# Performance work log

Hardware: AMD Instinct MI355X
Metric: run time of the kernel (lower is better)

## Reference

```python
import jax, jax.numpy as jnp
import numpy as np

B, S, HID = 2, 2048, 2048
H, KV, D = 16, 8, 128
EPS = 1e-6
MROPE = [21, 21, 22]  # half_dim=64 -> [64//3, 64//3, 64-2*(64//3)]
SCALE = D ** -0.5


def setup_inputs() -> dict:
    key = jax.random.key(0)
    ks = jax.random.split(key, 8)
    hidden_states = jax.random.normal(ks[0], (B, S, HID), jnp.float32)
    # 3D mrope cos/sin: one position grid per modality axis (use same arange positions)
    inv_freq = 1.0 / (10000.0 ** (jnp.arange(0, D, 2, dtype=jnp.float32) / D))  # [64]
    pos = jnp.arange(S, dtype=jnp.float32)
    freqs = pos[:, None] * inv_freq[None, :]                  # [S, 64]
    emb = jnp.concatenate([freqs, freqs], axis=-1)            # [S, 128]
    cos = jnp.broadcast_to(jnp.cos(emb)[None, None], (3, B, S, D)).astype(jnp.float32)
    sin = jnp.broadcast_to(jnp.sin(emb)[None, None], (3, B, S, D)).astype(jnp.float32)
    q_w = jax.random.normal(ks[1], (H * D, HID), jnp.float32) * 0.02
    k_w = jax.random.normal(ks[2], (KV * D, HID), jnp.float32) * 0.02
    v_w = jax.random.normal(ks[3], (KV * D, HID), jnp.float32) * 0.02
    o_w = jax.random.normal(ks[4], (HID, H * D), jnp.float32) * 0.02
    q_norm_w = jnp.ones((D,), jnp.float32)
    k_norm_w = jnp.ones((D,), jnp.float32)
    return dict(hidden_states=hidden_states, cos=cos, sin=sin, q_w=q_w, k_w=k_w,
                v_w=v_w, o_w=o_w, q_norm_w=q_norm_w, k_norm_w=k_norm_w)


def _rmsnorm(x, w):
    var = jnp.mean(jnp.square(x.astype(jnp.float32)), axis=-1, keepdims=True)
    return (x * jax.lax.rsqrt(var + EPS)).astype(x.dtype) * w


def _rotate_half(x):
    x1, x2 = jnp.split(x, 2, axis=-1)
    return jnp.concatenate([-x2, x1], axis=-1)


def _mrope_mix(t):
    # t: [3, B, S, D]; split last dim into mrope_section*2 chunks, pick chunk i from axis-0 index i%3
    sections = MROPE * 2
    idx = np.cumsum(sections)[:-1]
    chunks = jnp.split(t, idx, axis=-1)
    mixed = jnp.concatenate([c[i % 3] for i, c in enumerate(chunks)], axis=-1)  # [B, S, D]
    return mixed[:, None, :, :]  # unsqueeze head dim -> [B, 1, S, D]


def reference(hidden_states, cos, sin, q_w, k_w, v_w, o_w, q_norm_w, k_norm_w):
    # QKV projections -> [B, n_heads, S, D]
    q = (hidden_states @ q_w.T).reshape(B, S, H, D)
    k = (hidden_states @ k_w.T).reshape(B, S, KV, D)
    v = (hidden_states @ v_w.T).reshape(B, S, KV, D)
    q = _rmsnorm(q, q_norm_w).transpose(0, 2, 1, 3)   # [B, H, S, D]
    k = _rmsnorm(k, k_norm_w).transpose(0, 2, 1, 3)   # [B, KV, S, D]
    v = v.transpose(0, 2, 1, 3)                       # [B, KV, S, D]
    # 3D multimodal RoPE
    c = _mrope_mix(cos)
    s = _mrope_mix(sin)
    q = q * c + _rotate_half(q) * s
    k = k * c + _rotate_half(k) * s
    # GQA: repeat kv heads
    groups = H // KV
    k = jnp.repeat(k, groups, axis=1)  # [B, H, S, D]
    v = jnp.repeat(v, groups, axis=1)
    # causal SDPA (eager)
    scores = jnp.einsum('bhqd,bhkd->bhqk', q, k) * SCALE
    causal = jnp.tril(jnp.ones((S, S), bool))
    scores = jnp.where(causal[None, None], scores, jnp.finfo(scores.dtype).min)
    probs = jax.nn.softmax(scores, axis=-1)
    attn = jnp.einsum('bhqk,bhkd->bhqd', probs, v)     # [B, H, S, D]
    attn = attn.transpose(0, 2, 1, 3).reshape(B, S, H * D)
    return attn @ o_w.T
```

## Files before the change

kernel.cpp:

```cpp
#include <hip/hip_runtime.h>
#include <hip/hip_bf16.h>

typedef __attribute__((ext_vector_type(8))) short short8;
typedef __attribute__((ext_vector_type(4))) short short4v;
typedef __attribute__((ext_vector_type(4))) float f32x4;

#define B_ 2
#define S_ 2048
#define HID_ 2048
#define H_ 16
#define KV_ 8
#define D_ 128
#define SCALE_ 0.08838834764831845f

__device__ inline short f2bf(float f) {
    union { __hip_bfloat16 h; short s; } u;
    u.h = __float2bfloat16(f);
    return u.s;
}
__device__ inline float bf2f(short s) {
    union { short s; __hip_bfloat16 h; } u;
    u.s = s;
    return __bfloat162float(u.h);
}

__device__ inline void gld16(const short* g, short* l) {
    __builtin_amdgcn_global_load_lds(
        (const __attribute__((address_space(1))) unsigned int*)g,
        (__attribute__((address_space(3))) unsigned int*)l, 16, 0, 0);
}

__device__ inline int mrope_axis(int d) {
    int m = d & 63;
    return m < 21 ? 0 : (m < 42 ? 1 : 2);
}
__global__ __launch_bounds__(256) void prep(const float* __restrict__ hid,
                                            const float* __restrict__ qw_,
                                            const float* __restrict__ kw_,
                                            const float* __restrict__ vw_,
                                            const float* __restrict__ ow_,
                                            const float* __restrict__ cosp,
                                            const float* __restrict__ sinp,
                                            short* __restrict__ Hb,
                                            short* __restrict__ Wqkv,
                                            short* __restrict__ Owb,
                                            float* __restrict__ cm,
                                            float* __restrict__ sm) {
    int bid = blockIdx.x;
    if (bid < 20480) {
        const float* src; short* dst; int base;
        if (bid < 8192)       { src = hid; dst = Hb;              base = bid; }
        else if (bid < 12288) { src = qw_; dst = Wqkv;            base = bid - 8192; }
        else if (bid < 14336) { src = kw_; dst = Wqkv + 4194304;  base = bid - 12288; }
        else if (bid < 16384) { src = vw_; dst = Wqkv + 6291456;  base = bid - 14336; }
        else                  { src = ow_; dst = Owb;             base = bid - 16384; }
        int i = base * 1024 + threadIdx.x * 4;
        float4 v = *(const float4*)(&src[i]);
        short4v o;
        o.x = f2bf(v.x); o.y = f2bf(v.y); o.z = f2bf(v.z); o.w = f2bf(v.w);
        *(short4v*)(&dst[i]) = o;
    } else {
        const size_t AX = (size_t)B_ * S_ * D_;
        int i0 = (bid - 20480) * 1024 + threadIdx.x * 4;
#pragma unroll
        for (int k = 0; k < 4; ++k) {
            int idx = i0 + k;
            int d = idx & (D_ - 1);
            size_t src = (size_t)mrope_axis(d) * AX + idx;
            cm[idx] = cosp[src];
            sm[idx] = sinp[src];
        }
    }
}

__global__ __launch_bounds__(256) void gemm_bt(const short* __restrict__ A,
                                               const short* __restrict__ B,
                                               float* __restrict__ C,
                                               int M, int N, int K) {
    __shared__ __align__(16) short As[128 * 64];
    __shared__ __align__(16) short Bs[128 * 64];
    int tid = threadIdx.x;
    int wave = tid >> 6, lane = tid & 63;
    int m16 = lane & 15, quad = lane >> 4;
    int wr = wave >> 1, wc = wave & 1;
    int m0 = blockIdx.y * 128, n0 = blockIdx.x * 128;
    int srow = lane >> 3;
    int scol = ((lane & 7) ^ srow) << 3;
    f32x4 acc[4][4] = {};
    for (int k0 = 0; k0 < K; k0 += 64) {
#pragma unroll
        for (int i = 0; i < 4; ++i) {
            gld16(&A[(size_t)(m0 + wave * 32 + i * 8 + srow) * K + k0 + scol],
                  &As[(wave * 32 + i * 8) * 64]);
            gld16(&B[(size_t)(n0 + wave * 32 + i * 8 + srow) * K + k0 + scol],
                  &Bs[(wave * 32 + i * 8) * 64]);
        }
        __syncthreads();
        short8 a[4][2], b[4][2];
#pragma unroll
        for (int i = 0; i < 4; ++i)
#pragma unroll
            for (int kk = 0; kk < 2; ++kk) {
                int gsw = (((kk << 2) + quad) ^ (m16 & 7)) << 3;
                a[i][kk] = *(const short8*)(&As[(wr * 64 + i * 16 + m16) * 64 + gsw]);
                b[i][kk] = *(const short8*)(&Bs[(wc * 64 + i * 16 + m16) * 64 + gsw]);
            }
#pragma unroll
        for (int kk = 0; kk < 2; ++kk)
#pragma unroll
            for (int i = 0; i < 4; ++i)
#pragma unroll
                for (int j = 0; j < 4; ++j)
                    acc[i][j] = __builtin_amdgcn_mfma_f32_16x16x32_bf16(a[i][kk], b[j][kk],
                                                                        acc[i][j], 0, 0, 0);
        __syncthreads();
    }
#pragma unroll
    for (int i = 0; i < 4; ++i) {
        int row = m0 + wr * 64 + i * 16 + quad * 4;
#pragma unroll
        for (int j = 0; j < 4; ++j) {
            int col = n0 + wc * 64 + j * 16 + m16;
#pragma unroll
            for (int r = 0; r < 4; ++r)
                C[(size_t)(row + r) * N + col] = acc[i][j][r];
        }
    }
}


#define VM2 asm volatile("s_waitcnt vmcnt(2)" ::: "memory")
#define VM0 asm volatile("s_waitcnt vmcnt(0)" ::: "memory")

#define LDA(dst, QI)                                                               \
    _Pragma("unroll") for (int ii = 0; ii < 4; ++ii)                               \
        _Pragma("unroll") for (int kk = 0; kk < 2; ++kk)                           \
            dst[ii][kk] = *(const short8*)&lds[RA +                                \
                (wr * 128 + ((QI) * 4 + ii) * 16 + m16) * 64 +                     \
                ((((kk << 2) + quad) ^ (m16 & 7)) << 3)]

#define LDB(dst, QJ)                                                               \
    _Pragma("unroll") for (int jj = 0; jj < 2; ++jj)                               \
        _Pragma("unroll") for (int kk = 0; kk < 2; ++kk)                           \
            dst[jj][kk] = *(const short8*)&lds[RB +                                \
                ((QJ) * 128 + wc * 32 + jj * 16 + m16) * 64 +                      \
                ((((kk << 2) + quad) ^ (m16 & 7)) << 3)]

#define MM(ua, ub, QI, QJ)                                                         \
    _Pragma("unroll") for (int kk = 0; kk < 2; ++kk)                               \
        _Pragma("unroll") for (int ii = 0; ii < 4; ++ii)                           \
            _Pragma("unroll") for (int jj = 0; jj < 2; ++jj)                       \
                acc[(QI) * 4 + ii][(QJ) * 2 + jj] =                                \
                    __builtin_amdgcn_mfma_f32_16x16x32_bf16(                       \
                        ua[ii][kk], ub[jj][kk],                                    \
                        acc[(QI) * 4 + ii][(QJ) * 2 + jj], 0, 0, 0)

#define STGA(q) do {                                                               \
    int r_ = (wave << 3) + (lane >> 3);                                            \
    int g_ = (lane & 7) ^ (r_ & 7);                                                \
    gld16(&Am[(size_t)(m0 + (q) * 64 + r_) * 2048 + kc + (g_ << 3)],               \
          &lds[PA + (q) * 4096 + (wave << 9)]);                                    \
} while (0)
#define STGB(h, c) do {                                                            \
    int s_ = (wave << 3) + (lane >> 3);                                            \
    int sl_ = (h) * 128 + (c) * 64 + s_;                                           \
    int rr_ = ((sl_ >> 5) & 3) * 64 + (h) * 32 + (sl_ & 31);                       \
    int g_ = (lane & 7) ^ (sl_ & 7);                                               \
    gld16(&Bm[(size_t)(n0 + rr_) * 2048 + kc + (g_ << 3)],                         \
          &lds[PB + ((h) * 128 + (c) * 64) * 64 + (wave << 9)]);                   \
} while (0)

#define PH(LOADS, STG, MFMAS, WAITOP) do {                                         \
    LOADS;                                                                         \
    STG;                                                                           \
    __builtin_amdgcn_sched_barrier(0);                                             \
    __builtin_amdgcn_s_barrier();                                                  \
    asm volatile("s_waitcnt lgkmcnt(0)" ::: "memory");                             \
    __builtin_amdgcn_sched_barrier(0);                                             \
    __builtin_amdgcn_s_setprio(1);                                                 \
    MFMAS;                                                                         \
    __builtin_amdgcn_s_setprio(0);                                                 \
    WAITOP;                                                                        \
    __builtin_amdgcn_sched_barrier(0);                                             \
    __builtin_amdgcn_s_barrier();                                                  \
} while (0)

__global__ __launch_bounds__(512, 2) void qkv_fused(const short* __restrict__ Am,
                                                    const short* __restrict__ Bm,
                                                    const float* __restrict__ qnw,
                                                    const float* __restrict__ knw,
                                                    const float* __restrict__ cm,
                                                    const float* __restrict__ sm,
                                                    short* __restrict__ Qb,
                                                    short* __restrict__ Kb,
                                                    short* __restrict__ Vb) {
    __shared__ __align__(16) char smem[131072];
    short* lds = (short*)smem;
    int tid = threadIdx.x;
    int wave = tid >> 6, lane = tid & 63;
    int m16 = lane & 15, quad = lane >> 4;
    int wr = wave >> 2, wc = wave & 3;
    int m0 = blockIdx.y * 256, n0 = blockIdx.x * 256;
    f32x4 acc[8][4] = {};

    {
        const int kc = 0, PA = 0, PB = 16384;
        STGA(0); STGA(1); STGA(2); STGA(3);
        STGB(0, 0); STGB(0, 1); STGB(1, 0); STGB(1, 1);
        asm volatile("s_waitcnt vmcnt(0)" ::: "memory");
        __builtin_amdgcn_sched_barrier(0);
        __builtin_amdgcn_s_barrier();
    }

    short8 af[4][2], bfX[2][2], bfY[2][2];
    for (int t = 0; t < 31; ++t) {
        const int RA = (t & 1) << 15, RB = RA + 16384;
        const int PA = RA ^ 32768, PB = PA + 16384;
        const int kc = (t + 1) << 6;
        PH({ LDA(af, 0); LDB(bfX, 0); }, { STGA(0); STGA(2); },       MM(af, bfX, 0, 0), VM2);
        PH({ LDB(bfY, 1); },             { STGB(0, 0); STGB(0, 1); }, MM(af, bfY, 0, 1), );
        PH({ LDA(af, 1); },              { STGB(1, 0); STGB(1, 1); }, MM(af, bfY, 1, 1), );
        PH({ ; },                        { STGA(1); STGA(3); },       MM(af, bfX, 1, 0), VM2);
    }
    {
        const int RA = 32768, RB = RA + 16384;
        PH({ LDA(af, 0); LDB(bfX, 0); }, { ; }, MM(af, bfX, 0, 0), VM0);
        PH({ LDB(bfY, 1); },             { ; }, MM(af, bfY, 0, 1), );
        PH({ LDA(af, 1); },              { ; }, MM(af, bfY, 1, 1), );
        PH({ ; },                        { ; }, MM(af, bfX, 1, 0), );
    }

    int bb = m0 >> 11, s0 = m0 & (S_ - 1);
    int x = blockIdx.x;
    if (x >= 12) {
        short* T = (short*)smem;
        int kv0 = (x - 12) << 1;
        for (int hs = 0; hs < 2; ++hs) {
            __syncthreads();
            if (wr == hs) {
#pragma unroll
                for (int i = 0; i < 8; ++i)
#pragma unroll
                    for (int j = 0; j < 4; ++j) {
                        short4v v4;
#pragma unroll
                        for (int r = 0; r < 4; ++r) v4[r] = f2bf(acc[i][j][r]);
                        *(short4v*)&T[(wc * 64 + j * 16 + m16) * 136 + i * 16 + quad * 4] = v4;
                    }
            }
            __syncthreads();
#pragma unroll
            for (int it = 0; it < 8; ++it) {
                int e = (it * 512 + tid) * 8;
                int col = e >> 7, ro = e & 127;
                int kvh = col >> 7, d = col & 127;
                *(short8*)&Vb[(((size_t)(bb * KV_ + kv0 + kvh)) * D_ + d) * S_ +
                              s0 + hs * 128 + ro] =
                    *(const short8*)&T[col * 136 + ro];
            }
        }
    } else {
        short* T = (short*)smem;
        float* part = (float*)(smem + 67584);
        float* rsL  = (float*)(smem + 69632);
        const float* nw = (x < 8) ? qnw : knw;
        int hbase = (x < 8) ? (x << 1) : ((x - 8) << 1);
        short* obase = (x < 8) ? (Qb + ((size_t)bb * H_ + hbase) * S_ * D_)
                               : (Kb + ((size_t)bb * KV_ + hbase) * S_ * D_);
        for (int hs = 0; hs < 2; ++hs) {
            __syncthreads();
            if (wr == hs) {
#pragma unroll
                for (int i = 0; i < 8; ++i)
#pragma unroll
                    for (int r = 0; r < 4; ++r) {
                        float t = acc[i][0][r] * acc[i][0][r] + acc[i][1][r] * acc[i][1][r]
                                + acc[i][2][r] * acc[i][2][r] + acc[i][3][r] * acc[i][3][r];
#pragma unroll
                        for (int msk = 8; msk >= 1; msk >>= 1) t += __shfl_xor(t, msk, 64);
                        if (m16 == 0) part[wc * 128 + i * 16 + quad * 4 + r] = t;
                    }
#pragma unroll
                for (int i = 0; i < 8; ++i)
#pragma unroll
                    for (int j = 0; j < 4; ++j)
#pragma unroll
                        for (int r = 0; r < 4; ++r)
                            T[(i * 16 + quad * 4 + r) * 264 + wc * 64 + j * 16 + m16] =
                                f2bf(acc[i][j][r]);
            }
            __syncthreads();
            if (tid < 256) {
                int row = tid >> 1, hh = tid & 1;
                float tot = part[hh * 256 + row] + part[hh * 256 + 128 + row];
                rsL[tid] = rsqrtf(tot * (1.0f / 128.0f) + 1e-6f);
            }
            __syncthreads();
#pragma unroll
            for (int it = 0; it < 8; ++it) {
                int e = (it * 512 + tid) * 8;
                int row = e >> 8, c = e & 255;
                int hh = c >> 7, colc = c & 127;
                int pcol = colc ^ 64;
                int srow = s0 + hs * 128 + row;
                float rsv = rsL[row * 2 + hh];
                float sg = (colc < 64) ? -1.f : 1.f;
                short8 nv = *(const short8*)&T[row * 264 + c];
                short8 pv = *(const short8*)&T[row * 264 + hh * 128 + pcol];
                size_t cmb = ((size_t)(bb * S_ + srow)) * D_ + colc;
                float4 cA = *(const float4*)&cm[cmb];
                float4 cB = *(const float4*)&cm[cmb + 4];
                float4 sA = *(const float4*)&sm[cmb];
                float4 sB = *(const float4*)&sm[cmb + 4];
                float4 wA = *(const float4*)&nw[colc];
                float4 wB = *(const float4*)&nw[colc + 4];
                float4 wpA = *(const float4*)&nw[pcol];
                float4 wpB = *(const float4*)&nw[pcol + 4];
                float cs[8] = {cA.x, cA.y, cA.z, cA.w, cB.x, cB.y, cB.z, cB.w};
                float sn[8] = {sA.x, sA.y, sA.z, sA.w, sB.x, sB.y, sB.z, sB.w};
                float wv[8] = {wA.x, wA.y, wA.z, wA.w, wB.x, wB.y, wB.z, wB.w};
                float wp[8] = {wpA.x, wpA.y, wpA.z, wpA.w, wpB.x, wpB.y, wpB.z, wpB.w};
                short8 o;
#pragma unroll
                for (int k = 0; k < 8; ++k) {
                    float xv = bf2f(nv[k]) * rsv * wv[k];
                    float pvv = bf2f(pv[k]) * rsv * wp[k];
                    o[k] = f2bf(xv * cs[k] + sg * pvv * sn[k]);
                }
                *(short8*)&(obase + (size_t)hh * S_ * D_)[(size_t)srow * D_ + colc] = o;
            }
        }
    }
}

#undef PH
#undef LDA
#undef LDB
#undef MM
#undef STGA
#undef STGB
#undef VM2
#undef VM0

#define KPAD 136
#define VPAD 72
__global__ __launch_bounds__(256) void attn_fa(const short* __restrict__ Qb,
                                               const short* __restrict__ Kb,
                                               const short* __restrict__ Vb,
                                               short* __restrict__ Ab) {
    __shared__ __align__(16) short Ks[64 * KPAD];
    __shared__ __align__(16) short Vs[128 * VPAD];
    __shared__ __align__(16) short Ps[4][16 * VPAD];
    int tid = threadIdx.x;
    int wave = tid >> 6, lane = tid & 63;
    int m16 = lane & 15, quad = lane >> 4;
    int bh = blockIdx.x;
    int h = bh & 15, b = bh >> 4;
    int qt = 31 - blockIdx.y;
    int kv = h >> 1;
    const short* Qp = Qb + (size_t)(b * H_ + h) * S_ * D_;
    const short* Kp = Kb + (size_t)(b * KV_ + kv) * S_ * D_;
    const short* Vp = Vb + (size_t)(b * KV_ + kv) * D_ * S_;
    int q_base = qt * 64 + wave * 16;
    int qrow = q_base + m16;
    short8 qf[4];
#pragma unroll
    for (int c = 0; c < 4; ++c)
        qf[c] = *(const short8*)(&Qp[(size_t)(q_base + m16) * D_ + c * 32 + quad * 8]);
    f32x4 o_acc[8] = {};
    float m_r = -1e30f, l_r = 0.f;
    int nchunks = qt + 1;
    for (int kc = 0; kc < nchunks; ++kc) {
        int k0 = kc * 64;
#pragma unroll
        for (int it = 0; it < 4; ++it) {
            int cc = tid + it * 256;
            int row = cc >> 4, col = (cc & 15) * 8;
            *(uint4*)(&Ks[row * KPAD + col]) = *(const uint4*)(&Kp[(size_t)(k0 + row) * D_ + col]);
        }
#pragma unroll
        for (int it = 0; it < 4; ++it) {
            int cc = tid + it * 256;
            int row = cc >> 3, col = (cc & 7) * 8;
            *(uint4*)(&Vs[row * VPAD + col]) = *(const uint4*)(&Vp[(size_t)row * S_ + k0 + col]);
        }
        __syncthreads();
        float sv[4][4];
#pragma unroll
        for (int nt = 0; nt < 4; ++nt) {
            f32x4 facc = {};
#pragma unroll
            for (int c = 0; c < 4; ++c) {
                short8 kfr = *(const short8*)(&Ks[(nt * 16 + m16) * KPAD + c * 32 + quad * 8]);
                facc = __builtin_amdgcn_mfma_f32_16x16x32_bf16(kfr, qf[c], facc, 0, 0, 0);
            }
            if (kc == qt) {
#pragma unroll
                for (int r = 0; r < 4; ++r) {
                    int key = k0 + nt * 16 + quad * 4 + r;
                    sv[nt][r] = (key <= qrow) ? facc[r] * SCALE_ : -1e30f;
                }
            } else {
#pragma unroll
                for (int r = 0; r < 4; ++r) sv[nt][r] = facc[r] * SCALE_;
            }
        }
        float mx = -1e30f;
#pragma unroll
        for (int nt = 0; nt < 4; ++nt)
#pragma unroll
            for (int r = 0; r < 4; ++r) mx = fmaxf(mx, sv[nt][r]);
        mx = fmaxf(mx, __shfl_xor(mx, 16, 64));
        mx = fmaxf(mx, __shfl_xor(mx, 32, 64));
        float m_new = fmaxf(m_r, mx);
        float alpha = __expf(m_r - m_new);
        float p[4][4], sum = 0.f;
#pragma unroll
        for (int nt = 0; nt < 4; ++nt)
#pragma unroll
            for (int r = 0; r < 4; ++r) { p[nt][r] = __expf(sv[nt][r] - m_new); sum += p[nt][r]; }
        sum += __shfl_xor(sum, 16, 64);
        sum += __shfl_xor(sum, 32, 64);
        l_r = l_r * alpha + sum;
        m_r = m_new;
#pragma unroll
        for (int j = 0; j < 8; ++j) {
            f32x4 t = o_acc[j];
#pragma unroll
            for (int r = 0; r < 4; ++r) t[r] *= alpha;
            o_acc[j] = t;
        }
#pragma unroll
        for (int nt = 0; nt < 4; ++nt) {
            short4v pk;
#pragma unroll
            for (int r = 0; r < 4; ++r) pk[r] = f2bf(p[nt][r]);
            *(short4v*)&Ps[wave][m16 * VPAD + nt * 16 + quad * 4] = pk;
        }
#pragma unroll
        for (int kk = 0; kk < 2; ++kk) {
            short8 pf = *(const short8*)(&Ps[wave][m16 * VPAD + kk * 32 + quad * 8]);
#pragma unroll
            for (int j = 0; j < 8; ++j) {
                short8 vfr = *(const short8*)(&Vs[(j * 16 + m16) * VPAD + kk * 32 + quad * 8]);
                o_acc[j] = __builtin_amdgcn_mfma_f32_16x16x32_bf16(vfr, pf, o_acc[j], 0, 0, 0);
            }
        }
        __syncthreads();
    }
    float inv_l = 1.0f / l_r;
    size_t base = ((size_t)(b * S_ + qrow)) * (H_ * D_) + h * D_;
#pragma unroll
    for (int j = 0; j < 8; ++j) {
        short4v ov;
#pragma unroll
        for (int r = 0; r < 4; ++r) ov[r] = f2bf(o_acc[j][r] * inv_l);
        *(short4v*)&Ab[base + j * 16 + quad * 4] = ov;
    }
}

extern "C" void kernel_launch(void* const* d_in, const int* in_sizes, int n_in,
                              void* d_out, int out_size, void* d_ws, size_t ws_size,
                              hipStream_t stream) {
    const float* hid  = (const float*)d_in[0];
    const float* cosp = (const float*)d_in[1];
    const float* sinp = (const float*)d_in[2];
    const float* q_w  = (const float*)d_in[3];
    const float* k_w  = (const float*)d_in[4];
    const float* v_w  = (const float*)d_in[5];
    const float* o_w  = (const float*)d_in[6];
    const float* qnw  = (const float*)d_in[7];
    const float* knw  = (const float*)d_in[8];

    char* w = (char*)d_ws;
    short* Hb    = (short*)w;  w += (size_t)4096 * 2048 * 2;
    short* Wqkv  = (short*)w;  w += (size_t)4096 * 2048 * 2;
    short* Owb   = (short*)w;  w += (size_t)2048 * 2048 * 2;
    short* Qb    = (short*)w;  w += (size_t)B_ * H_ * S_ * D_ * 2;
    short* Kb    = (short*)w;  w += (size_t)B_ * KV_ * S_ * D_ * 2;
    short* Vb    = (short*)w;  w += (size_t)B_ * KV_ * D_ * S_ * 2;
    short* Ab    = (short*)w;  w += (size_t)4096 * 2048 * 2;
    float* cos_m = (float*)w;  w += (size_t)B_ * S_ * D_ * 4;
    float* sin_m = (float*)w;  w += (size_t)B_ * S_ * D_ * 4;

    prep<<<20992, 256, 0, stream>>>(hid, q_w, k_w, v_w, o_w, cosp, sinp,
                                    Hb, Wqkv, Owb, cos_m, sin_m);

    qkv_fused<<<dim3(16, 16), 512, 0, stream>>>(Hb, Wqkv, qnw, knw, cos_m, sin_m,
                                                Qb, Kb, Vb);

    attn_fa<<<dim3(32, 32), 256, 0, stream>>>(Qb, Kb, Vb, Ab);

    gemm_bt<<<dim3(16, 32), 256, 0, stream>>>(Ab, Owb, (float*)d_out, 4096, 2048, 2048);
}
```

Before: 353.1 us.

## Split QKV epilogue into separate kernel, swizzle blocks, double-buffer attention K/V

The QKV GEMM no longer does RMSNorm and RoPE in its epilogue. It writes bf16 Q/K columns to a scratch buffer, and a new qkv_post kernel applies norm and rotary. The GEMM also gets a block-index swizzle for L2 locality, relaxed vmcnt waits, and drops the occupancy-2 launch bound. Attention now double-buffers K/V tiles with async global-to-LDS loads into XOR-swizzled LDS and raises priority around the MFMA sections. The tradeoff is an extra kernel launch and an extra write and read of a 4096x3072 intermediate.

After: 329.6 us. 6.7% less time.

```diff
diff --git a/kernel.cpp b/kernel.cpp
--- a/kernel.cpp
+++ b/kernel.cpp
@@ -129,6 +129,7 @@
 }
 
 
+#define VM4 asm volatile("s_waitcnt vmcnt(4)" ::: "memory")
 #define VM2 asm volatile("s_waitcnt vmcnt(2)" ::: "memory")
 #define VM0 asm volatile("s_waitcnt vmcnt(0)" ::: "memory")
 
@@ -185,29 +186,28 @@
     __builtin_amdgcn_s_barrier();                                                  \
 } while (0)
 
-__global__ __launch_bounds__(512, 2) void qkv_fused(const short* __restrict__ Am,
-                                                    const short* __restrict__ Bm,
-                                                    const float* __restrict__ qnw,
-                                                    const float* __restrict__ knw,
-                                                    const float* __restrict__ cm,
-                                                    const float* __restrict__ sm,
-                                                    short* __restrict__ Qb,
-                                                    short* __restrict__ Kb,
-                                                    short* __restrict__ Vb) {
+__global__ __launch_bounds__(512) void gemm_qkv(const short* __restrict__ Am,
+                                                const short* __restrict__ Bm,
+                                                short* __restrict__ Cq,
+                                                short* __restrict__ Vb) {
     __shared__ __align__(16) char smem[131072];
     short* lds = (short*)smem;
     int tid = threadIdx.x;
     int wave = tid >> 6, lane = tid & 63;
     int m16 = lane & 15, quad = lane >> 4;
     int wr = wave >> 2, wc = wave & 3;
-    int m0 = blockIdx.y * 256, n0 = blockIdx.x * 256;
+    int orig = blockIdx.y * 16 + blockIdx.x;
+    int swz = (orig & 7) * 32 + (orig >> 3);
+    int bx = swz & 15, by = swz >> 4;
+    int m0 = by * 256, n0 = bx * 256;
+    int x = bx;
     f32x4 acc[8][4] = {};
 
     {
         const int kc = 0, PA = 0, PB = 16384;
         STGA(0); STGA(1); STGA(2); STGA(3);
         STGB(0, 0); STGB(0, 1); STGB(1, 0); STGB(1, 1);
-        asm volatile("s_waitcnt vmcnt(0)" ::: "memory");
+        VM0;
         __builtin_amdgcn_sched_barrier(0);
         __builtin_amdgcn_s_barrier();
     }
@@ -217,21 +217,20 @@
         const int RA = (t & 1) << 15, RB = RA + 16384;
         const int PA = RA ^ 32768, PB = PA + 16384;
         const int kc = (t + 1) << 6;
-        PH({ LDA(af, 0); LDB(bfX, 0); }, { STGA(0); STGA(2); },       MM(af, bfX, 0, 0), VM2);
-        PH({ LDB(bfY, 1); },             { STGB(0, 0); STGB(0, 1); }, MM(af, bfY, 0, 1), );
-        PH({ LDA(af, 1); },              { STGB(1, 0); STGB(1, 1); }, MM(af, bfY, 1, 1), );
-        PH({ ; },                        { STGA(1); STGA(3); },       MM(af, bfX, 1, 0), VM2);
+        PH({ LDA(af, 0); LDB(bfX, 0); }, { STGA(0); STGA(2); },       MM(af, bfX, 0, 0), VM4);
+        PH({ LDB(bfY, 1); },             { STGB(0, 0); STGB(0, 1); }, MM(af, bfY, 0, 1), VM4);
+        PH({ LDA(af, 1); },              { STGB(1, 0); STGB(1, 1); }, MM(af, bfY, 1, 1), VM4);
+        PH({ ; },                        { STGA(1); STGA(3); },       MM(af, bfX, 1, 0), VM4);
     }
     {
         const int RA = 32768, RB = RA + 16384;
-        PH({ LDA(af, 0); LDB(bfX, 0); }, { ; }, MM(af, bfX, 0, 0), VM0);
-        PH({ LDB(bfY, 1); },             { ; }, MM(af, bfY, 0, 1), );
+        PH({ LDA(af, 0); LDB(bfX, 0); }, { ; }, MM(af, bfX, 0, 0), VM2);
+        PH({ LDB(bfY, 1); },             { ; }, MM(af, bfY, 0, 1), VM0);
         PH({ LDA(af, 1); },              { ; }, MM(af, bfY, 1, 1), );
         PH({ ; },                        { ; }, MM(af, bfX, 1, 0), );
     }
 
     int bb = m0 >> 11, s0 = m0 & (S_ - 1);
-    int x = blockIdx.x;
     if (x >= 12) {
         short* T = (short*)smem;
         int kv0 = (x - 12) << 1;
@@ -260,74 +259,15 @@
             }
         }
     } else {
-        short* T = (short*)smem;
-        float* part = (float*)(smem + 67584);
-        float* rsL  = (float*)(smem + 69632);
-        const float* nw = (x < 8) ? qnw : knw;
-        int hbase = (x < 8) ? (x << 1) : ((x - 8) << 1);
-        short* obase = (x < 8) ? (Qb + ((size_t)bb * H_ + hbase) * S_ * D_)
-                               : (Kb + ((size_t)bb * KV_ + hbase) * S_ * D_);
-        for (int hs = 0; hs < 2; ++hs) {
-            __syncthreads();
-            if (wr == hs) {
-#pragma unroll
-                for (int i = 0; i < 8; ++i)
-#pragma unroll
-                    for (int r = 0; r < 4; ++r) {
-                        float t = acc[i][0][r] * acc[i][0][r] + acc[i][1][r] * acc[i][1][r]
-                                + acc[i][2][r] * acc[i][2][r] + acc[i][3][r] * acc[i][3][r];
-#pragma unroll
-                        for (int msk = 8; msk >= 1; msk >>= 1) t += __shfl_xor(t, msk, 64);
-                        if (m16 == 0) part[wc * 128 + i * 16 + quad * 4 + r] = t;
-                    }
-#pragma unroll
-                for (int i = 0; i < 8; ++i)
-#pragma unroll
-                    for (int j = 0; j < 4; ++j)
-#pragma unroll
-                        for (int r = 0; r < 4; ++r)
-                            T[(i * 16 + quad * 4 + r) * 264 + wc * 64 + j * 16 + m16] =
-                                f2bf(acc[i][j][r]);
-            }
-            __syncthreads();
-            if (tid < 256) {
-                int row = tid >> 1, hh = tid & 1;
-                float tot = part[hh * 256 + row] + part[hh * 256 + 128 + row];
-                rsL[tid] = rsqrtf(tot * (1.0f / 128.0f) + 1e-6f);
-            }
-            __syncthreads();
-#pragma unroll
-            for (int it = 0; it < 8; ++it) {
-                int e = (it * 512 + tid) * 8;
-                int row = e >> 8, c = e & 255;
-                int hh = c >> 7, colc = c & 127;
-                int pcol = colc ^ 64;
-                int srow = s0 + hs * 128 + row;
-                float rsv = rsL[row * 2 + hh];
-                float sg = (colc < 64) ? -1.f : 1.f;
-                short8 nv = *(const short8*)&T[row * 264 + c];
-                short8 pv = *(const short8*)&T[row * 264 + hh * 128 + pcol];
-                size_t cmb = ((size_t)(bb * S_ + srow)) * D_ + colc;
-                float4 cA = *(const float4*)&cm[cmb];
-                float4 cB = *(const float4*)&cm[cmb + 4];
-                float4 sA = *(const float4*)&sm[cmb];
-                float4 sB = *(const float4*)&sm[cmb + 4];
-                float4 wA = *(const float4*)&nw[colc];
-                float4 wB = *(const float4*)&nw[colc + 4];
-                float4 wpA = *(const float4*)&nw[pcol];
-                float4 wpB = *(const float4*)&nw[pcol + 4];
-                float cs[8] = {cA.x, cA.y, cA.z, cA.w, cB.x, cB.y, cB.z, cB.w};
-                float sn[8] = {sA.x, sA.y, sA.z, sA.w, sB.x, sB.y, sB.z, sB.w};
-                float wv[8] = {wA.x, wA.y, wA.z, wA.w, wB.x, wB.y, wB.z, wB.w};
-                float wp[8] = {wpA.x, wpA.y, wpA.z, wpA.w, wpB.x, wpB.y, wpB.z, wpB.w};
-                short8 o;
-#pragma unroll
-                for (int k = 0; k < 8; ++k) {
-                    float xv = bf2f(nv[k]) * rsv * wv[k];
-                    float pvv = bf2f(pv[k]) * rsv * wp[k];
-                    o[k] = f2bf(xv * cs[k] + sg * pvv * sn[k]);
-                }
-                *(short8*)&(obase + (size_t)hh * S_ * D_)[(size_t)srow * D_ + colc] = o;
+#pragma unroll
+        for (int i = 0; i < 8; ++i) {
+            int row = m0 + wr * 128 + i * 16 + quad * 4;
+#pragma unroll
+            for (int j = 0; j < 4; ++j) {
+                int col = n0 + wc * 64 + j * 16 + m16;
+#pragma unroll
+                for (int r = 0; r < 4; ++r)
+                    Cq[(size_t)(row + r) * 3072 + col] = f2bf(acc[i][j][r]);
             }
         }
     }
@@ -339,17 +279,84 @@
 #undef MM
 #undef STGA
 #undef STGB
+#undef VM4
 #undef VM2
 #undef VM0
 
-#define KPAD 136
+#define TP 136
+__global__ __launch_bounds__(256) void qkv_post(const short* __restrict__ Cq,
+                                                const float* __restrict__ qnw,
+                                                const float* __restrict__ knw,
+                                                const float* __restrict__ cm,
+                                                const float* __restrict__ sm,
+                                                short* __restrict__ Qb,
+                                                short* __restrict__ Kb) {
+    __shared__ __align__(16) short T[128 * TP];
+    __shared__ float sq[128];
+    __shared__ float rsA[128];
+    int tid = threadIdx.x;
+    int hk = blockIdx.x;
+    int m0 = blockIdx.y * 128;
+    int b = m0 >> 11, s0 = m0 & (S_ - 1);
+#pragma unroll
+    for (int it = 0; it < 8; ++it) {
+        int idx = it * 256 + tid;
+        int row = idx >> 4, g = idx & 15;
+        short8 v = *(const short8*)&Cq[(size_t)(m0 + row) * 3072 + hk * 128 + g * 8];
+        *(short8*)&T[row * TP + g * 8] = v;
+        float s = 0.f;
+#pragma unroll
+        for (int k = 0; k < 8; ++k) { float f = bf2f(v[k]); s += f * f; }
+#pragma unroll
+        for (int msk = 8; msk >= 1; msk >>= 1) s += __shfl_xor(s, msk, 64);
+        if ((tid & 15) == 0) sq[row] = s;
+    }
+    __syncthreads();
+    if (tid < 128) rsA[tid] = rsqrtf(sq[tid] * (1.0f / 128.0f) + 1e-6f);
+    __syncthreads();
+    const float* nw = (hk < 16) ? qnw : knw;
+    short* outp = (hk < 16) ? (Qb + ((size_t)(b * H_ + hk)) * S_ * D_)
+                            : (Kb + ((size_t)(b * KV_ + hk - 16)) * S_ * D_);
+    size_t cmb = ((size_t)(b * S_ + s0)) * D_;
+#pragma unroll
+    for (int it = 0; it < 8; ++it) {
+        int e = (it * 256 + tid) * 8;
+        int row = e >> 7, colc = e & 127;
+        int pc = colc ^ 64;
+        float rs = rsA[row];
+        float sg = (colc < 64) ? -1.f : 1.f;
+        short8 nv = *(const short8*)&T[row * TP + colc];
+        short8 pv = *(const short8*)&T[row * TP + pc];
+        float4 cA = *(const float4*)&cm[cmb + (size_t)row * D_ + colc];
+        float4 cB = *(const float4*)&cm[cmb + (size_t)row * D_ + colc + 4];
+        float4 sA = *(const float4*)&sm[cmb + (size_t)row * D_ + colc];
+        float4 sB = *(const float4*)&sm[cmb + (size_t)row * D_ + colc + 4];
+        float4 wA = *(const float4*)&nw[colc];
+        float4 wB = *(const float4*)&nw[colc + 4];
+        float4 wpA = *(const float4*)&nw[pc];
+        float4 wpB = *(const float4*)&nw[pc + 4];
+        float cs[8] = {cA.x, cA.y, cA.z, cA.w, cB.x, cB.y, cB.z, cB.w};
+        float sn[8] = {sA.x, sA.y, sA.z, sA.w, sB.x, sB.y, sB.z, sB.w};
+        float wv[8] = {wA.x, wA.y, wA.z, wA.w, wB.x, wB.y, wB.z, wB.w};
+        float wp[8] = {wpA.x, wpA.y, wpA.z, wpA.w, wpB.x, wpB.y, wpB.z, wpB.w};
+        short8 o;
+#pragma unroll
+        for (int k = 0; k < 8; ++k) {
+            float xv = bf2f(nv[k]) * rs * wv[k];
+            float pvv = bf2f(pv[k]) * rs * wp[k];
+            o[k] = f2bf(xv * cs[k] + sg * pvv * sn[k]);
+        }
+        *(short8*)&outp[(size_t)(s0 + row) * D_ + colc] = o;
+    }
+}
+
 #define VPAD 72
 __global__ __launch_bounds__(256) void attn_fa(const short* __restrict__ Qb,
                                                const short* __restrict__ Kb,
                                                const short* __restrict__ Vb,
                                                short* __restrict__ Ab) {
-    __shared__ __align__(16) short Ks[64 * KPAD];
-    __shared__ __align__(16) short Vs[128 * VPAD];
+    __shared__ __align__(16) short Ks[2][64 * 128];
+    __shared__ __align__(16) short Vs[2][128 * 64];
     __shared__ __align__(16) short Ps[4][16 * VPAD];
     int tid = threadIdx.x;
     int wave = tid >> 6, lane = tid & 63;
@@ -370,28 +377,52 @@
     f32x4 o_acc[8] = {};
     float m_r = -1e30f, l_r = 0.f;
     int nchunks = qt + 1;
+
+#pragma unroll
+    for (int j = 0; j < 4; ++j) {
+        int idx = wave * 4 + j;
+        int r = idx * 4 + (lane >> 4);
+        int g = (lane & 15) ^ (r & 7);
+        gld16(&Kp[(size_t)r * D_ + g * 8], &Ks[0][idx * 512]);
+    }
+#pragma unroll
+    for (int j = 0; j < 4; ++j) {
+        int idx = wave * 4 + j;
+        int r = idx * 8 + (lane >> 3);
+        int g = (lane & 7) ^ (r & 7);
+        gld16(&Vp[(size_t)r * S_ + g * 8], &Vs[0][idx * 512]);
+    }
+    __syncthreads();
+
     for (int kc = 0; kc < nchunks; ++kc) {
         int k0 = kc * 64;
-#pragma unroll
-        for (int it = 0; it < 4; ++it) {
-            int cc = tid + it * 256;
-            int row = cc >> 4, col = (cc & 15) * 8;
-            *(uint4*)(&Ks[row * KPAD + col]) = *(const uint4*)(&Kp[(size_t)(k0 + row) * D_ + col]);
-        }
-#pragma unroll
-        for (int it = 0; it < 4; ++it) {
-            int cc = tid + it * 256;
-            int row = cc >> 3, col = (cc & 7) * 8;
-            *(uint4*)(&Vs[row * VPAD + col]) = *(const uint4*)(&Vp[(size_t)row * S_ + k0 + col]);
-        }
-        __syncthreads();
+        int cur = kc & 1;
+        if (kc + 1 < nchunks) {
+            int nk0 = k0 + 64, nb = cur ^ 1;
+#pragma unroll
+            for (int j = 0; j < 4; ++j) {
+                int idx = wave * 4 + j;
+                int r = idx * 4 + (lane >> 4);
+                int g = (lane & 15) ^ (r & 7);
+                gld16(&Kp[(size_t)(nk0 + r) * D_ + g * 8], &Ks[nb][idx * 512]);
+            }
+#pragma unroll
+            for (int j = 0; j < 4; ++j) {
+                int idx = wave * 4 + j;
+                int r = idx * 8 + (lane >> 3);
+                int g = (lane & 7) ^ (r & 7);
+                gld16(&Vp[(size_t)r * S_ + nk0 + g * 8], &Vs[nb][idx * 512]);
+            }
+        }
         float sv[4][4];
+        __builtin_amdgcn_s_setprio(1);
 #pragma unroll
         for (int nt = 0; nt < 4; ++nt) {
             f32x4 facc = {};
 #pragma unroll
             for (int c = 0; c < 4; ++c) {
-                short8 kfr = *(const short8*)(&Ks[(nt * 16 + m16) * KPAD + c * 32 + quad * 8]);
+                short8 kfr = *(const short8*)(&Ks[cur][(nt * 16 + m16) * 128 +
+                                                      ((((c << 2) + quad) ^ (m16 & 7)) << 3)]);
                 facc = __builtin_amdgcn_mfma_f32_16x16x32_bf16(kfr, qf[c], facc, 0, 0, 0);
             }
             if (kc == qt) {
@@ -405,6 +436,7 @@
                 for (int r = 0; r < 4; ++r) sv[nt][r] = facc[r] * SCALE_;
             }
         }
+        __builtin_amdgcn_s_setprio(0);
         float mx = -1e30f;
 #pragma unroll
         for (int nt = 0; nt < 4; ++nt)
@@ -424,28 +456,31 @@
         l_r = l_r * alpha + sum;
         m_r = m_new;
 #pragma unroll
+        for (int nt = 0; nt < 4; ++nt) {
+            short4v pk;
+#pragma unroll
+            for (int r = 0; r < 4; ++r) pk[r] = f2bf(p[nt][r]);
+            *(short4v*)&Ps[wave][m16 * VPAD + nt * 16 + quad * 4] = pk;
+        }
+#pragma unroll
         for (int j = 0; j < 8; ++j) {
             f32x4 t = o_acc[j];
 #pragma unroll
             for (int r = 0; r < 4; ++r) t[r] *= alpha;
             o_acc[j] = t;
         }
-#pragma unroll
-        for (int nt = 0; nt < 4; ++nt) {
-            short4v pk;
-#pragma unroll
-            for (int r = 0; r < 4; ++r) pk[r] = f2bf(p[nt][r]);
-            *(short4v*)&Ps[wave][m16 * VPAD + nt * 16 + quad * 4] = pk;
-        }
+        __builtin_amdgcn_s_setprio(1);
 #pragma unroll
         for (int kk = 0; kk < 2; ++kk) {
             short8 pf = *(const short8*)(&Ps[wave][m16 * VPAD + kk * 32 + quad * 8]);
 #pragma unroll
             for (int j = 0; j < 8; ++j) {
-                short8 vfr = *(const short8*)(&Vs[(j * 16 + m16) * VPAD + kk * 32 + quad * 8]);
+                short8 vfr = *(const short8*)(&Vs[cur][(j * 16 + m16) * 64 +
+                                                       ((((kk << 2) + quad) ^ (m16 & 7)) << 3)]);
                 o_acc[j] = __builtin_amdgcn_mfma_f32_16x16x32_bf16(vfr, pf, o_acc[j], 0, 0, 0);
             }
         }
+        __builtin_amdgcn_s_setprio(0);
         __syncthreads();
     }
     float inv_l = 1.0f / l_r;
@@ -482,12 +517,14 @@
     short* Ab    = (short*)w;  w += (size_t)4096 * 2048 * 2;
     float* cos_m = (float*)w;  w += (size_t)B_ * S_ * D_ * 4;
     float* sin_m = (float*)w;  w += (size_t)B_ * S_ * D_ * 4;
+    short* Cq    = (short*)w;  w += (size_t)4096 * 3072 * 2;
 
     prep<<<20992, 256, 0, stream>>>(hid, q_w, k_w, v_w, o_w, cosp, sinp,
                                     Hb, Wqkv, Owb, cos_m, sin_m);
 
-    qkv_fused<<<dim3(16, 16), 512, 0, stream>>>(Hb, Wqkv, qnw, knw, cos_m, sin_m,
-                                                Qb, Kb, Vb);
+    gemm_qkv<<<dim3(16, 16), 512, 0, stream>>>(Hb, Wqkv, Cq, Vb);
+
+    qkv_post<<<dim3(24, 32), 256, 0, stream>>>(Cq, qnw, knw, cos_m, sin_m, Qb, Kb);
 
     attn_fa<<<dim3(32, 32), 256, 0, stream>>>(Qb, Kb, Vb, Ab);
 
```
